# Performance work log

Measured on AMD Instinct MI355X. Metric: run time of the kernel, lower is better.

The kernel has to match this reference:

```python
import jax, jax.numpy as jnp
import numpy as np

NUM_FIELDS = 26
VOCAB = 100000
B = 16384
D = 64            # embedding_dim
BM1, BM2 = 128, 64    # bottom_mlp_sizes
TM1, TM2 = 256, 1     # top mlp hidden/out (top_mlp_sizes=[512,256,1] -> Linear(415,256),ReLU,Linear(256,1))
NUM_FEATS = NUM_FIELDS + 1
NUM_INTER = NUM_FEATS * (NUM_FEATS - 1) // 2   # 351
TOP_IN = NUM_INTER + BM2                        # 415


def setup_inputs() -> dict:
    key = jax.random.key(0)
    ks = jax.random.split(key, 13)
    x_cat = jax.random.randint(ks[0], (NUM_FIELDS, B), 0, VOCAB)
    price = jax.random.normal(ks[1], (B,), dtype=jnp.float32)
    emb_tables = jax.random.normal(ks[2], (NUM_FIELDS, VOCAB, D), dtype=jnp.float32) * 0.05
    Wp = jax.random.normal(ks[3], (1, D), dtype=jnp.float32) * 0.1
    bp = jnp.zeros((D,), jnp.float32)
    W1 = jax.random.normal(ks[4], (D, BM1), dtype=jnp.float32) * 0.1
    b1 = jnp.zeros((BM1,), jnp.float32)
    W2 = jax.random.normal(ks[5], (BM1, BM2), dtype=jnp.float32) * 0.1
    b2 = jnp.zeros((BM2,), jnp.float32)
    Wt1 = jax.random.normal(ks[6], (TOP_IN, TM1), dtype=jnp.float32) * 0.05
    bt1 = jnp.zeros((TM1,), jnp.float32)
    Wt2 = jax.random.normal(ks[7], (TM1, TM2), dtype=jnp.float32) * 0.05
    bt2 = jnp.zeros((TM2,), jnp.float32)
    return {"x_cat": x_cat, "price": price, "emb_tables": emb_tables,
            "Wp": Wp, "bp": bp, "W1": W1, "b1": b1, "W2": W2, "b2": b2,
            "Wt1": Wt1, "bt1": bt1, "Wt2": Wt2, "bt2": bt2}


# precomputed upper-triangular (i<j, row-major) index pairs -- matches the torch double loop order
_IU, _JU = np.triu_indices(NUM_FEATS, k=1)


def reference(x_cat, price, emb_tables, Wp, bp, W1, b1, W2, b2, Wt1, bt1, Wt2, bt2):
    # embedding gathers: [F, B, D] -> [B, F, D]
    emb = emb_tables[jnp.arange(NUM_FIELDS)[:, None], x_cat]
    emb = jnp.transpose(emb, (1, 0, 2))
    # dense (price) projection: [B, D]
    dense_embed = price[:, None] @ Wp + bp
    # all features: [B, F+1, D]
    feats = jnp.concatenate([emb, dense_embed[:, None, :]], axis=1)
    # pairwise dot products via batched Gram matrix, then triangular gather
    gram = jnp.einsum('bid,bjd->bij', feats, feats)          # [B, 27, 27]
    interactions = gram[:, _IU, _JU]                          # [B, 351]
    # bottom MLP on dense embedding
    h = jax.nn.relu(dense_embed @ W1 + b1)
    dense_out = jax.nn.relu(h @ W2 + b2)                      # [B, 64]
    # top MLP
    concat = jnp.concatenate([interactions, dense_out], axis=1)  # [B, 415]
    t = jax.nn.relu(concat @ Wt1 + bt1)
    out = (t @ Wt2 + bt2)[:, 0]                               # [B]
    return out
```

## Files before the change

### kernel.cpp

```cpp
#include <hip/hip_runtime.h>
#include <hip/hip_bf16.h>
#include <cstdint>

#define NUM_FIELDS 26
#define VOCAB      100000
#define BATCH      16384
#define CONCAT_K   416
#define TOPN       256

typedef __attribute__((ext_vector_type(8)))  short bf16x8_t;
typedef __attribute__((ext_vector_type(16))) float f32x16_t;

__device__ __forceinline__ short f2bf(float x) {
  unsigned u = __builtin_bit_cast(unsigned, x);
  u += 0x7FFFu + ((u >> 16) & 1u);
  return (short)(u >> 16);
}

__global__ void k0_prepare(const float* __restrict__ Wp, const float* __restrict__ bp,
                           const float* __restrict__ W1, const float* __restrict__ b1,
                           const float* __restrict__ W2, const float* __restrict__ b2,
                           float* __restrict__ bps, float* __restrict__ PQ) {
  __shared__ float u1s[128], c1s[128], ts[128];
  __shared__ int ord[128];
  const int j = threadIdx.x;
  float u = 0.f, c = 0.f;
  for (int d = 0; d < 64; ++d) {
    float w = W1[d * 128 + j];
    u = fmaf(Wp[d], w, u);
    c = fmaf(bp[d], w, c);
  }
  c += b1[j];
  u1s[j] = u; c1s[j] = c;
  ts[j] = (u != 0.f) ? (-c / u) : __builtin_inff();
  __syncthreads();
  const float tj = ts[j];
  int r = 0;
  for (int i = 0; i < 128; ++i) {
    float ti = ts[i];
    if (ti < tj || (ti == tj && i < j)) ++r;
  }
  ord[r] = j;
  __syncthreads();
  bps[j] = ts[ord[j]];
  if (j < 64) {
    const int d = j;
    float P = 0.f, Q = b2[d];
    for (int k = 0; k < 128; ++k) {
      float uk = u1s[k];
      bool act = (uk < 0.f) || (uk == 0.f && c1s[k] > 0.f);
      if (act) {
        float w = W2[k * 64 + d];
        P = fmaf(uk, w, P);
        Q = fmaf(c1s[k], w, Q);
      }
    }
    PQ[d] = P; PQ[129 * 64 + d] = Q;
    for (int seg = 1; seg <= 128; ++seg) {
      int jk = ord[seg - 1];
      float uk = u1s[jk], ck = c1s[jk];
      float sgn = (uk > 0.f) ? 1.f : ((uk < 0.f) ? -1.f : 0.f);
      float w = W2[jk * 64 + d] * sgn;
      P = fmaf(uk, w, P);
      Q = fmaf(ck, w, Q);
      PQ[seg * 64 + d] = P;
      PQ[129 * 64 + seg * 64 + d] = Q;
    }
  }
}

__global__ __launch_bounds__(256) void k1_features(
    const int* __restrict__ x_cat, const float* __restrict__ price,
    const float* __restrict__ emb, const float* __restrict__ Wp,
    const float* __restrict__ bp, const float* __restrict__ bps_g,
    const float* __restrict__ PQ, float* __restrict__ concat) {
  __shared__ __align__(16) short Fb[4][32 * 72];
  __shared__ float bps_s[128];
  const int tid = threadIdx.x, lane = tid & 63, w = tid >> 6;
  if (tid < 128) bps_s[tid] = bps_g[tid];
  {
    int* zp = (int*)&Fb[w][27 * 72];
    for (int i = lane; i < 180; i += 64) zp[i] = 0;
  }
  __syncthreads();
  const float wp = Wp[lane], bpv = bp[lane];
  const int gw = blockIdx.x * 4 + w;
  const int row = lane & 31, koff = (lane >> 5) * 8;
  for (int it = 0; it < 8; ++it) {
    const int s = gw * 8 + it;
    const float pr = price[s];
    #pragma unroll
    for (int f = 0; f < NUM_FIELDS; ++f) {
      int idx = x_cat[f * BATCH + s];
      float v = emb[(size_t)(f * VOCAB + idx) * 64 + lane];
      Fb[w][f * 72 + lane] = f2bf(v);
    }
    Fb[w][26 * 72 + lane] = f2bf(fmaf(pr, wp, bpv));
    __syncthreads();
    bf16x8_t a0 = *(const bf16x8_t*)&Fb[w][row * 72 +  0 + koff];
    bf16x8_t a1 = *(const bf16x8_t*)&Fb[w][row * 72 + 16 + koff];
    bf16x8_t a2 = *(const bf16x8_t*)&Fb[w][row * 72 + 32 + koff];
    bf16x8_t a3 = *(const bf16x8_t*)&Fb[w][row * 72 + 48 + koff];
    f32x16_t acc = {0.f,0.f,0.f,0.f,0.f,0.f,0.f,0.f,0.f,0.f,0.f,0.f,0.f,0.f,0.f,0.f};
    acc = __builtin_amdgcn_mfma_f32_32x32x16_bf16(a0, a0, acc, 0, 0, 0);
    acc = __builtin_amdgcn_mfma_f32_32x32x16_bf16(a1, a1, acc, 0, 0, 0);
    acc = __builtin_amdgcn_mfma_f32_32x32x16_bf16(a2, a2, acc, 0, 0, 0);
    acc = __builtin_amdgcn_mfma_f32_32x32x16_bf16(a3, a3, acc, 0, 0, 0);
    int lo = 0, hi = 128;
    while (lo < hi) { int mid = (lo + hi) >> 1; if (bps_s[mid] < pr) lo = mid + 1; else hi = mid; }
    float dv = fmaf(pr, PQ[lo * 64 + lane], PQ[129 * 64 + lo * 64 + lane]);
    dv = fmaxf(dv, 0.f);
    float* cb = concat + (size_t)s * CONCAT_K;
    cb[351 + lane] = dv;
    if (lane == 0) cb[415] = 0.f;
    const int jcol = row;
    const int rh = (lane >> 5) * 4;
    #pragma unroll
    for (int reg = 0; reg < 16; ++reg) {
      int i = (reg & 3) + 8 * (reg >> 2) + rh;
      if (i < jcol && jcol < 27) {
        int p = 26 * i - (i * (i - 1)) / 2 + (jcol - i - 1);
        cb[p] = acc[reg];
      }
    }
    __syncthreads();
  }
}

__global__ __launch_bounds__(256) void k2_gemm(const float* __restrict__ concat,
                                               const float* __restrict__ Wt1,
                                               float* __restrict__ Cp) {
  __shared__ float As[32][132];
  __shared__ float Bs[32][264];
  const int tid = threadIdx.x;
  const int tx = tid & 15, ty = tid >> 4;
  const int m0 = blockIdx.x * 128;
  const int kb = blockIdx.y;
  const int k0 = kb ? 224 : 0;
  const int nch = kb ? 6 : 7;
  float acc[8][16];
  #pragma unroll
  for (int i = 0; i < 8; ++i)
    #pragma unroll
    for (int n = 0; n < 16; ++n) acc[i][n] = 0.f;
  const int k4 = tid & 7, mrow = tid >> 3;
  const int kq = tid >> 6, n4 = tid & 63;
  for (int ch = 0; ch < nch; ++ch) {
    const int kc = k0 + ch * 32;
    #pragma unroll
    for (int rr = 0; rr < 4; ++rr) {
      const int m = mrow + rr * 32;
      float4 a = *(const float4*)&concat[(size_t)(m0 + m) * CONCAT_K + kc + k4 * 4];
      As[k4 * 4 + 0][m] = a.x;
      As[k4 * 4 + 1][m] = a.y;
      As[k4 * 4 + 2][m] = a.z;
      As[k4 * 4 + 3][m] = a.w;
    }
    #pragma unroll
    for (int rr = 0; rr < 8; ++rr) {
      const int k = rr * 4 + kq;
      float4 b = make_float4(0.f, 0.f, 0.f, 0.f);
      if (kc + k < 415) b = *(const float4*)&Wt1[(size_t)(kc + k) * 256 + n4 * 4];
      *(float4*)&Bs[k][n4 * 4] = b;
    }
    __syncthreads();
    #pragma unroll 4
    for (int k = 0; k < 32; ++k) {
      float av[8], bv[16];
      float4 a0 = *(const float4*)&As[k][ty * 8];
      float4 a1 = *(const float4*)&As[k][ty * 8 + 4];
      av[0]=a0.x; av[1]=a0.y; av[2]=a0.z; av[3]=a0.w;
      av[4]=a1.x; av[5]=a1.y; av[6]=a1.z; av[7]=a1.w;
      #pragma unroll
      for (int q = 0; q < 4; ++q) {
        float4 bq = *(const float4*)&Bs[k][q * 64 + tx * 4];
        bv[q*4+0]=bq.x; bv[q*4+1]=bq.y; bv[q*4+2]=bq.z; bv[q*4+3]=bq.w;
      }
      #pragma unroll
      for (int i = 0; i < 8; ++i)
        #pragma unroll
        for (int n = 0; n < 16; ++n)
          acc[i][n] = fmaf(av[i], bv[n], acc[i][n]);
    }
    __syncthreads();
  }
  #pragma unroll
  for (int i = 0; i < 8; ++i) {
    size_t ro = ((size_t)kb * BATCH + m0 + ty * 8 + i) * 256;
    #pragma unroll
    for (int q = 0; q < 4; ++q) {
      float4 v = make_float4(acc[i][q*4+0], acc[i][q*4+1], acc[i][q*4+2], acc[i][q*4+3]);
      *(float4*)&Cp[ro + q * 64 + tx * 4] = v;
    }
  }
}

__global__ __launch_bounds__(256) void k3_out(const float* __restrict__ Cp,
                                              const float* __restrict__ bt1,
                                              const float* __restrict__ Wt2,
                                              const float* __restrict__ bt2,
                                              float* __restrict__ out) {
  const int tid = threadIdx.x, lane = tid & 63, w = tid >> 6;
  const int s = blockIdx.x * 4 + w;
  const float4 c0 = *(const float4*)&Cp[(size_t)s * 256 + lane * 4];
  const float4 c1 = *(const float4*)&Cp[(size_t)(BATCH + s) * 256 + lane * 4];
  const float4 bb = *(const float4*)&bt1[lane * 4];
  const float4 w2 = *(const float4*)&Wt2[lane * 4];
  float sum = fmaxf(c0.x + c1.x + bb.x, 0.f) * w2.x
            + fmaxf(c0.y + c1.y + bb.y, 0.f) * w2.y
            + fmaxf(c0.z + c1.z + bb.z, 0.f) * w2.z
            + fmaxf(c0.w + c1.w + bb.w, 0.f) * w2.w;
  #pragma unroll
  for (int off = 32; off > 0; off >>= 1) sum += __shfl_down(sum, off, 64);
  if (lane == 0) out[s] = sum + bt2[0];
}

extern "C" void kernel_launch(void* const* d_in, const int* in_sizes, int n_in,
                              void* d_out, int out_size, void* d_ws, size_t ws_size,
                              hipStream_t stream) {
  const int*   x_cat = (const int*)d_in[0];
  const float* price = (const float*)d_in[1];
  const float* emb   = (const float*)d_in[2];
  const float* Wp    = (const float*)d_in[3];
  const float* bp    = (const float*)d_in[4];
  const float* W1    = (const float*)d_in[5];
  const float* b1    = (const float*)d_in[6];
  const float* W2    = (const float*)d_in[7];
  const float* b2    = (const float*)d_in[8];
  const float* Wt1   = (const float*)d_in[9];
  const float* bt1   = (const float*)d_in[10];
  const float* Wt2   = (const float*)d_in[11];
  const float* bt2   = (const float*)d_in[12];
  float* out = (float*)d_out;

  float* ws     = (float*)d_ws;
  float* PQ     = ws;
  float* bps    = ws + 16512;
  float* concat = ws + 16640;
  float* Cp     = concat + (size_t)BATCH * CONCAT_K;

  k0_prepare<<<dim3(1), dim3(128), 0, stream>>>(Wp, bp, W1, b1, W2, b2, bps, PQ);
  k1_features<<<dim3(512), dim3(256), 0, stream>>>(x_cat, price, emb, Wp, bp, bps, PQ, concat);
  k2_gemm<<<dim3(128, 2), dim3(256), 0, stream>>>(concat, Wt1, Cp);
  k3_out<<<dim3(BATCH / 4), dim3(256), 0, stream>>>(Cp, bt1, Wt2, bt2, out);
}
```

Measured before the change: 898.0 us.

## Replace fp32 top GEMM with bf16 MFMA fused with output layer, store concat as bf16

The concat intermediate is now stored as bf16 and written through a shared-memory staging buffer with coalesced 16-byte stores. The feature kernel handles one sample per wave with float4 gathers and shuffled indices, giving a much larger grid. The fp32 SIMT top GEMM and the separate output kernel are replaced by a bf16 MFMA kernel over a pre-transposed bf16 Wt1. That kernel fuses bias, ReLU and the final dot product, which removes the split-K partial buffer and its round trip through memory. The cost is lower precision in the top layer inputs and weights.

```diff
diff --git a/kernel.cpp b/kernel.cpp
--- a/kernel.cpp
+++ b/kernel.cpp
@@ -5,8 +5,7 @@
 #define NUM_FIELDS 26
 #define VOCAB      100000
 #define BATCH      16384
-#define CONCAT_K   416
-#define TOPN       256
+#define CK         416
 
 typedef __attribute__((ext_vector_type(8)))  short bf16x8_t;
 typedef __attribute__((ext_vector_type(16))) float f32x16_t;
@@ -69,12 +68,22 @@
   }
 }
 
+__global__ __launch_bounds__(64) void k0b_wt1t(const float* __restrict__ Wt1,
+                                               short* __restrict__ wt1t) {
+  const int n = blockIdx.x;
+  for (int k = threadIdx.x; k < CK; k += 64) {
+    float v = (k < 415) ? Wt1[(size_t)k * 256 + n] : 0.f;
+    wt1t[(size_t)n * CK + k] = f2bf(v);
+  }
+}
+
 __global__ __launch_bounds__(256) void k1_features(
     const int* __restrict__ x_cat, const float* __restrict__ price,
     const float* __restrict__ emb, const float* __restrict__ Wp,
     const float* __restrict__ bp, const float* __restrict__ bps_g,
-    const float* __restrict__ PQ, float* __restrict__ concat) {
+    const float* __restrict__ PQ, short* __restrict__ concat) {
   __shared__ __align__(16) short Fb[4][32 * 72];
+  __shared__ __align__(16) short Cs[4][CK];
   __shared__ float bps_s[128];
   const int tid = threadIdx.x, lane = tid & 63, w = tid >> 6;
   if (tid < 128) bps_s[tid] = bps_g[tid];
@@ -82,137 +91,110 @@
     int* zp = (int*)&Fb[w][27 * 72];
     for (int i = lane; i < 180; i += 64) zp[i] = 0;
   }
-  __syncthreads();
-  const float wp = Wp[lane], bpv = bp[lane];
-  const int gw = blockIdx.x * 4 + w;
+  const int s = blockIdx.x * 4 + w;
+  const float pr = price[s];
+  int idxv = 0;
+  if (lane < NUM_FIELDS) idxv = x_cat[lane * BATCH + s];
+  const int r16 = lane >> 4, c4 = (lane & 15) * 4;
+  #pragma unroll
+  for (int g = 0; g < 6; ++g) {
+    const int r = g * 4 + r16;
+    const int idx = __shfl(idxv, r, 64);
+    const float4 v = *(const float4*)&emb[((size_t)r * VOCAB + idx) * 64 + c4];
+    union { short s4[4]; uint2 u; } t;
+    t.s4[0] = f2bf(v.x); t.s4[1] = f2bf(v.y); t.s4[2] = f2bf(v.z); t.s4[3] = f2bf(v.w);
+    *(uint2*)&Fb[w][r * 72 + c4] = t.u;
+  }
+  {
+    const int r = 24 + ((lane >> 4) & 1);
+    const int idx = __shfl(idxv, r, 64);
+    if (lane < 32) {
+      const float4 v = *(const float4*)&emb[((size_t)r * VOCAB + idx) * 64 + c4];
+      union { short s4[4]; uint2 u; } t;
+      t.s4[0] = f2bf(v.x); t.s4[1] = f2bf(v.y); t.s4[2] = f2bf(v.z); t.s4[3] = f2bf(v.w);
+      *(uint2*)&Fb[w][r * 72 + c4] = t.u;
+    }
+  }
+  Fb[w][26 * 72 + lane] = f2bf(fmaf(pr, Wp[lane], bp[lane]));
+  __syncthreads();
   const int row = lane & 31, koff = (lane >> 5) * 8;
-  for (int it = 0; it < 8; ++it) {
-    const int s = gw * 8 + it;
-    const float pr = price[s];
+  bf16x8_t a0 = *(const bf16x8_t*)&Fb[w][row * 72 +  0 + koff];
+  bf16x8_t a1 = *(const bf16x8_t*)&Fb[w][row * 72 + 16 + koff];
+  bf16x8_t a2 = *(const bf16x8_t*)&Fb[w][row * 72 + 32 + koff];
+  bf16x8_t a3 = *(const bf16x8_t*)&Fb[w][row * 72 + 48 + koff];
+  f32x16_t acc = {0.f,0.f,0.f,0.f,0.f,0.f,0.f,0.f,0.f,0.f,0.f,0.f,0.f,0.f,0.f,0.f};
+  acc = __builtin_amdgcn_mfma_f32_32x32x16_bf16(a0, a0, acc, 0, 0, 0);
+  acc = __builtin_amdgcn_mfma_f32_32x32x16_bf16(a1, a1, acc, 0, 0, 0);
+  acc = __builtin_amdgcn_mfma_f32_32x32x16_bf16(a2, a2, acc, 0, 0, 0);
+  acc = __builtin_amdgcn_mfma_f32_32x32x16_bf16(a3, a3, acc, 0, 0, 0);
+  int lo = 0, hi = 128;
+  while (lo < hi) { int mid = (lo + hi) >> 1; if (bps_s[mid] < pr) lo = mid + 1; else hi = mid; }
+  float dv = fmaf(pr, PQ[lo * 64 + lane], PQ[129 * 64 + lo * 64 + lane]);
+  dv = fmaxf(dv, 0.f);
+  Cs[w][351 + lane] = f2bf(dv);
+  if (lane == 0) Cs[w][415] = 0;
+  const int jc = row, rh = (lane >> 5) * 4;
+  #pragma unroll
+  for (int reg = 0; reg < 16; ++reg) {
+    int i = (reg & 3) + 8 * (reg >> 2) + rh;
+    if (i < jc && jc < 27) {
+      int p = 26 * i - (i * (i - 1)) / 2 + (jc - i - 1);
+      Cs[w][p] = f2bf(acc[reg]);
+    }
+  }
+  __syncthreads();
+  if (lane < 52) {
+    *(uint4*)&concat[(size_t)s * CK + lane * 8] = ((const uint4*)Cs[w])[lane];
+  }
+}
+
+__global__ __launch_bounds__(256) void k2_top(const short* __restrict__ concat,
+    const short* __restrict__ wt1t, const float* __restrict__ bt1,
+    const float* __restrict__ Wt2, const float* __restrict__ bt2,
+    float* __restrict__ out) {
+  __shared__ float partial_s[4][32];
+  const int tid = threadIdx.x, lane = tid & 63, w = tid >> 6;
+  const int m0 = blockIdx.x * 32;
+  const int row = lane & 31, kh = lane >> 5;
+  const short* ap  = concat + (size_t)(m0 + row) * CK + kh * 8;
+  const int nb = w * 64;
+  const short* bp0 = wt1t + (size_t)(nb + row) * CK + kh * 8;
+  const short* bp1 = bp0 + (size_t)32 * CK;
+  f32x16_t acc0 = {0.f,0.f,0.f,0.f,0.f,0.f,0.f,0.f,0.f,0.f,0.f,0.f,0.f,0.f,0.f,0.f};
+  f32x16_t acc1 = acc0;
+  #pragma unroll
+  for (int k0 = 0; k0 < CK; k0 += 16) {
+    bf16x8_t a  = *(const bf16x8_t*)(ap + k0);
+    bf16x8_t b0 = *(const bf16x8_t*)(bp0 + k0);
+    bf16x8_t b1 = *(const bf16x8_t*)(bp1 + k0);
+    acc0 = __builtin_amdgcn_mfma_f32_32x32x16_bf16(a, b0, acc0, 0, 0, 0);
+    acc1 = __builtin_amdgcn_mfma_f32_32x32x16_bf16(a, b1, acc1, 0, 0, 0);
+  }
+  const int n0 = nb + row;
+  const float bt1a = bt1[n0], bt1b = bt1[n0 + 32];
+  const float w2a  = Wt2[n0], w2b  = Wt2[n0 + 32];
+  float ps[16];
+  #pragma unroll
+  for (int r = 0; r < 16; ++r) {
+    float v0 = fmaxf(acc0[r] + bt1a, 0.f) * w2a;
+    float v1 = fmaxf(acc1[r] + bt1b, 0.f) * w2b;
+    ps[r] = v0 + v1;
+  }
+  #pragma unroll
+  for (int d = 1; d <= 16; d <<= 1) {
     #pragma unroll
-    for (int f = 0; f < NUM_FIELDS; ++f) {
-      int idx = x_cat[f * BATCH + s];
-      float v = emb[(size_t)(f * VOCAB + idx) * 64 + lane];
-      Fb[w][f * 72 + lane] = f2bf(v);
-    }
-    Fb[w][26 * 72 + lane] = f2bf(fmaf(pr, wp, bpv));
-    __syncthreads();
-    bf16x8_t a0 = *(const bf16x8_t*)&Fb[w][row * 72 +  0 + koff];
-    bf16x8_t a1 = *(const bf16x8_t*)&Fb[w][row * 72 + 16 + koff];
-    bf16x8_t a2 = *(const bf16x8_t*)&Fb[w][row * 72 + 32 + koff];
-    bf16x8_t a3 = *(const bf16x8_t*)&Fb[w][row * 72 + 48 + koff];
-    f32x16_t acc = {0.f,0.f,0.f,0.f,0.f,0.f,0.f,0.f,0.f,0.f,0.f,0.f,0.f,0.f,0.f,0.f};
-    acc = __builtin_amdgcn_mfma_f32_32x32x16_bf16(a0, a0, acc, 0, 0, 0);
-    acc = __builtin_amdgcn_mfma_f32_32x32x16_bf16(a1, a1, acc, 0, 0, 0);
-    acc = __builtin_amdgcn_mfma_f32_32x32x16_bf16(a2, a2, acc, 0, 0, 0);
-    acc = __builtin_amdgcn_mfma_f32_32x32x16_bf16(a3, a3, acc, 0, 0, 0);
-    int lo = 0, hi = 128;
-    while (lo < hi) { int mid = (lo + hi) >> 1; if (bps_s[mid] < pr) lo = mid + 1; else hi = mid; }
-    float dv = fmaf(pr, PQ[lo * 64 + lane], PQ[129 * 64 + lo * 64 + lane]);
-    dv = fmaxf(dv, 0.f);
-    float* cb = concat + (size_t)s * CONCAT_K;
-    cb[351 + lane] = dv;
-    if (lane == 0) cb[415] = 0.f;
-    const int jcol = row;
-    const int rh = (lane >> 5) * 4;
+    for (int r = 0; r < 16; ++r) ps[r] += __shfl_xor(ps[r], d, 64);
+  }
+  if (row == 0) {
+    const int rh = kh * 4;
     #pragma unroll
-    for (int reg = 0; reg < 16; ++reg) {
-      int i = (reg & 3) + 8 * (reg >> 2) + rh;
-      if (i < jcol && jcol < 27) {
-        int p = 26 * i - (i * (i - 1)) / 2 + (jcol - i - 1);
-        cb[p] = acc[reg];
-      }
-    }
-    __syncthreads();
-  }
-}
-
-__global__ __launch_bounds__(256) void k2_gemm(const float* __restrict__ concat,
-                                               const float* __restrict__ Wt1,
-                                               float* __restrict__ Cp) {
-  __shared__ float As[32][132];
-  __shared__ float Bs[32][264];
-  const int tid = threadIdx.x;
-  const int tx = tid & 15, ty = tid >> 4;
-  const int m0 = blockIdx.x * 128;
-  const int kb = blockIdx.y;
-  const int k0 = kb ? 224 : 0;
-  const int nch = kb ? 6 : 7;
-  float acc[8][16];
-  #pragma unroll
-  for (int i = 0; i < 8; ++i)
-    #pragma unroll
-    for (int n = 0; n < 16; ++n) acc[i][n] = 0.f;
-  const int k4 = tid & 7, mrow = tid >> 3;
-  const int kq = tid >> 6, n4 = tid & 63;
-  for (int ch = 0; ch < nch; ++ch) {
-    const int kc = k0 + ch * 32;
-    #pragma unroll
-    for (int rr = 0; rr < 4; ++rr) {
-      const int m = mrow + rr * 32;
-      float4 a = *(const float4*)&concat[(size_t)(m0 + m) * CONCAT_K + kc + k4 * 4];
-      As[k4 * 4 + 0][m] = a.x;
-      As[k4 * 4 + 1][m] = a.y;
-      As[k4 * 4 + 2][m] = a.z;
-      As[k4 * 4 + 3][m] = a.w;
-    }
-    #pragma unroll
-    for (int rr = 0; rr < 8; ++rr) {
-      const int k = rr * 4 + kq;
-      float4 b = make_float4(0.f, 0.f, 0.f, 0.f);
-      if (kc + k < 415) b = *(const float4*)&Wt1[(size_t)(kc + k) * 256 + n4 * 4];
-      *(float4*)&Bs[k][n4 * 4] = b;
-    }
-    __syncthreads();
-    #pragma unroll 4
-    for (int k = 0; k < 32; ++k) {
-      float av[8], bv[16];
-      float4 a0 = *(const float4*)&As[k][ty * 8];
-      float4 a1 = *(const float4*)&As[k][ty * 8 + 4];
-      av[0]=a0.x; av[1]=a0.y; av[2]=a0.z; av[3]=a0.w;
-      av[4]=a1.x; av[5]=a1.y; av[6]=a1.z; av[7]=a1.w;
-      #pragma unroll
-      for (int q = 0; q < 4; ++q) {
-        float4 bq = *(const float4*)&Bs[k][q * 64 + tx * 4];
-        bv[q*4+0]=bq.x; bv[q*4+1]=bq.y; bv[q*4+2]=bq.z; bv[q*4+3]=bq.w;
-      }
-      #pragma unroll
-      for (int i = 0; i < 8; ++i)
-        #pragma unroll
-        for (int n = 0; n < 16; ++n)
-          acc[i][n] = fmaf(av[i], bv[n], acc[i][n]);
-    }
-    __syncthreads();
-  }
-  #pragma unroll
-  for (int i = 0; i < 8; ++i) {
-    size_t ro = ((size_t)kb * BATCH + m0 + ty * 8 + i) * 256;
-    #pragma unroll
-    for (int q = 0; q < 4; ++q) {
-      float4 v = make_float4(acc[i][q*4+0], acc[i][q*4+1], acc[i][q*4+2], acc[i][q*4+3]);
-      *(float4*)&Cp[ro + q * 64 + tx * 4] = v;
-    }
-  }
-}
-
-__global__ __launch_bounds__(256) void k3_out(const float* __restrict__ Cp,
-                                              const float* __restrict__ bt1,
-                                              const float* __restrict__ Wt2,
-                                              const float* __restrict__ bt2,
-                                              float* __restrict__ out) {
-  const int tid = threadIdx.x, lane = tid & 63, w = tid >> 6;
-  const int s = blockIdx.x * 4 + w;
-  const float4 c0 = *(const float4*)&Cp[(size_t)s * 256 + lane * 4];
-  const float4 c1 = *(const float4*)&Cp[(size_t)(BATCH + s) * 256 + lane * 4];
-  const float4 bb = *(const float4*)&bt1[lane * 4];
-  const float4 w2 = *(const float4*)&Wt2[lane * 4];
-  float sum = fmaxf(c0.x + c1.x + bb.x, 0.f) * w2.x
-            + fmaxf(c0.y + c1.y + bb.y, 0.f) * w2.y
-            + fmaxf(c0.z + c1.z + bb.z, 0.f) * w2.z
-            + fmaxf(c0.w + c1.w + bb.w, 0.f) * w2.w;
-  #pragma unroll
-  for (int off = 32; off > 0; off >>= 1) sum += __shfl_down(sum, off, 64);
-  if (lane == 0) out[s] = sum + bt2[0];
+    for (int r = 0; r < 16; ++r)
+      partial_s[w][(r & 3) + 8 * (r >> 2) + rh] = ps[r];
+  }
+  __syncthreads();
+  if (tid < 32)
+    out[m0 + tid] = partial_s[0][tid] + partial_s[1][tid] +
+                    partial_s[2][tid] + partial_s[3][tid] + bt2[0];
 }
 
 extern "C" void kernel_launch(void* const* d_in, const int* in_sizes, int n_in,
@@ -236,11 +218,11 @@
   float* ws     = (float*)d_ws;
   float* PQ     = ws;
   float* bps    = ws + 16512;
-  float* concat = ws + 16640;
-  float* Cp     = concat + (size_t)BATCH * CONCAT_K;
-
-  k0_prepare<<<dim3(1), dim3(128), 0, stream>>>(Wp, bp, W1, b1, W2, b2, bps, PQ);
-  k1_features<<<dim3(512), dim3(256), 0, stream>>>(x_cat, price, emb, Wp, bp, bps, PQ, concat);
-  k2_gemm<<<dim3(128, 2), dim3(256), 0, stream>>>(concat, Wt1, Cp);
-  k3_out<<<dim3(BATCH / 4), dim3(256), 0, stream>>>(Cp, bt1, Wt2, bt2, out);
-}
+  short* concat = (short*)(ws + 16640);
+  short* wt1t   = concat + (size_t)BATCH * CK;
+
+  k0_prepare<<<dim3(1),   dim3(128), 0, stream>>>(Wp, bp, W1, b1, W2, b2, bps, PQ);
+  k0b_wt1t  <<<dim3(256), dim3(64),  0, stream>>>(Wt1, wt1t);
+  k1_features<<<dim3(BATCH / 4), dim3(256), 0, stream>>>(x_cat, price, emb, Wp, bp, bps, PQ, concat);
+  k2_top     <<<dim3(BATCH / 32), dim3(256), 0, stream>>>(concat, wt1t, bt1, Wt2, bt2, out);
+}
```

After: 826.1 us. -8.0%, faster.
